# Optimization experiments

Hardware: AMD Instinct MI355X
Metric: run time of the kernel (lower is better)

Reference implementation:

```python
import jax, jax.numpy as jnp
import numpy as np

D_MODEL = 1024
D_OUT = 1024
N_EXPERTS = 8
TOP_K = 2


def setup_inputs() -> dict:
    key = jax.random.key(0)
    ks = jax.random.split(key, 5)
    b, t = 4, 4096
    inputs = jax.random.normal(ks[0], (b, t, D_MODEL), dtype=jnp.float32)
    # gate: Linear(input_dim, num_experts) -> weight (E, d), bias (E,)
    Wg = jax.random.normal(ks[1], (N_EXPERTS, D_MODEL), dtype=jnp.float32) / np.sqrt(D_MODEL)
    bg = jnp.zeros((N_EXPERTS,), dtype=jnp.float32)
    # experts: E x Linear(input_dim, output_dim) -> (E, d, f) and (E, f)
    We = jax.random.normal(ks[2], (N_EXPERTS, D_MODEL, D_OUT), dtype=jnp.float32) / np.sqrt(D_MODEL)
    be = jnp.zeros((N_EXPERTS, D_OUT), dtype=jnp.float32)
    return {"inputs": inputs, "Wg": Wg, "bg": bg, "We": We, "be": be}


def reference(inputs, Wg, bg, We, be):
    # gate logits: (b, t, E)
    gate_logits = jnp.einsum('btd,ed->bte', inputs, Wg) + bg
    # top-k per token (values descending, distinct indices) -> (b, t, k)
    topv, topi = jax.lax.top_k(gate_logits, TOP_K)
    gatew = jax.nn.sigmoid(topv).astype(inputs.dtype)            # (b, t, k)
    # scatter the k gate weights into a dense per-expert combine weight (b, t, E)
    onehot = jax.nn.one_hot(topi, N_EXPERTS, dtype=inputs.dtype)  # (b, t, k, E)
    combine = jnp.einsum('btk,btke->bte', gatew, onehot)          # (b, t, E)
    # per-expert linear outputs for all tokens: (b, t, E, f)
    expert_out = jnp.einsum('btd,edf->btef', inputs, We) + be
    # weighted combine over experts (unselected experts have weight 0)
    results = jnp.einsum('bte,btef->btf', combine, expert_out)
    return results
```

## Files before the change

kernel.cpp:

```cpp
#include <hip/hip_runtime.h>
#include <math.h>

#define DM 1024
#define DF 1024
#define NE 8
#define NBIN 16
#define MAXT 136
#define BM 128
#define BN 64
#define BKT 32
#define NT 32

typedef __bf16 bf16x8 __attribute__((ext_vector_type(8)));
typedef __bf16 bf16x4 __attribute__((ext_vector_type(4)));
typedef float floatx4 __attribute__((ext_vector_type(4)));

typedef const __attribute__((address_space(1))) unsigned int* gas_t;
typedef __attribute__((address_space(3))) unsigned int* las_t;

__device__ __forceinline__ void ld_lds16(const void* g, void* l) {
    __builtin_amdgcn_global_load_lds((gas_t)g, (las_t)l, 16, 0, 0);
}

#define WAITVM(N) asm volatile("s_waitcnt vmcnt(" #N ")" ::: "memory")
#define BARRIER() do { asm volatile("" ::: "memory"); \
                       __builtin_amdgcn_s_barrier(); \
                       asm volatile("" ::: "memory"); } while (0)


__global__ void convert_weT(const float* __restrict__ We, __bf16* __restrict__ WeT) {
    int n  = blockIdx.x * 256 + threadIdx.x;
    int kc = blockIdx.y * 8;
    int e  = blockIdx.z;
    const float* src = We + ((size_t)e << 20) + (size_t)kc * DF + n;
    bf16x8 v;
#pragma unroll
    for (int j = 0; j < 8; ++j) v[j] = (__bf16)src[(size_t)j * DF];
    *(bf16x8*)&WeT[((size_t)e << 20) + (size_t)n * DM + kc] = v;
}

__global__ void gate_kernel(const float4* __restrict__ X4, const float4* __restrict__ Wg4,
                            const float* __restrict__ bg, int* __restrict__ tok_e,
                            float* __restrict__ tok_w, __bf16* __restrict__ Xb, int T) {
    int wid  = threadIdx.x >> 6;
    int lane = threadIdx.x & 63;
    int t = blockIdx.x * 4 + wid;
    if (t >= T) return;
    float acc[NE] = {};
    float4 xs[4];
#pragma unroll
    for (int c = 0; c < 4; ++c) {
        float4 xv = X4[(size_t)t * 256 + c * 64 + lane];
        xs[c] = xv;
#pragma unroll
        for (int e = 0; e < NE; ++e) {
            float4 wv = Wg4[e * 256 + c * 64 + lane];
            acc[e] += xv.x * wv.x + xv.y * wv.y + xv.z * wv.z + xv.w * wv.w;
        }
    }
#pragma unroll
    for (int c = 0; c < 4; ++c) {
        bf16x4 v;
        v[0] = (__bf16)xs[c].x; v[1] = (__bf16)xs[c].y;
        v[2] = (__bf16)xs[c].z; v[3] = (__bf16)xs[c].w;
        *(bf16x4*)&Xb[(size_t)t * DM + c * 256 + lane * 4] = v;
    }
#pragma unroll
    for (int e = 0; e < NE; ++e) {
#pragma unroll
        for (int off = 32; off > 0; off >>= 1)
            acc[e] += __shfl_down(acc[e], off, 64);
    }
    if (lane == 0) {
        float l[NE];
#pragma unroll
        for (int e = 0; e < NE; ++e) l[e] = acc[e] + bg[e];
        int b0 = 0; float v0 = l[0];
        for (int e = 1; e < NE; ++e) if (l[e] > v0) { v0 = l[e]; b0 = e; }
        int b1 = -1; float v1 = -3.4e38f;
        for (int e = 0; e < NE; ++e) if (e != b0 && l[e] > v1) { v1 = l[e]; b1 = e; }
        tok_e[2 * t]     = b0;  tok_e[2 * t + 1] = b1;
        tok_w[2 * t]     = 1.f / (1.f + expf(-v0));
        tok_w[2 * t + 1] = 1.f / (1.f + expf(-v1));
    }
}

__global__ void hist_kernel(const int* __restrict__ tok_e, int* __restrict__ blk_cnt, int n) {
    int b = blockIdx.x, tid = threadIdx.x;
    int idx  = b * 256 + tid;
    int lane = tid & 63, w = tid >> 6;
    int bin = (idx < n) ? ((idx & 1) * NE + tok_e[idx]) : -1;
    __shared__ int wc[4][NBIN];
#pragma unroll
    for (int bx = 0; bx < NBIN; ++bx) {
        unsigned long long m = __ballot(bin == bx);
        if (lane == 0) wc[w][bx] = (int)__popcll(m);
    }
    __syncthreads();
    if (tid < NBIN) blk_cnt[b * NBIN + tid] = wc[0][tid] + wc[1][tid] + wc[2][tid] + wc[3][tid];
}

__global__ void scan_kernel(const int* __restrict__ blk_cnt, int* __restrict__ blk_base,
                            int4* __restrict__ wl, int* __restrict__ ntiles, int NB) {
    __shared__ int c[2048];
    __shared__ int tot[NBIN], base[NBIN];
    int tid = threadIdx.x;
    for (int i = tid; i < NB * NBIN; i += 256) c[i] = blk_cnt[i];
    __syncthreads();
    if (tid < NBIN) {
        int s = 0;
        for (int b = 0; b < NB; ++b) s += c[b * NBIN + tid];
        tot[tid] = s;
    }
    __syncthreads();
    if (tid == 0) {
        int s = 0;
        for (int b = 0; b < NBIN; ++b) { base[b] = s; s += tot[b]; }
    }
    __syncthreads();
    if (tid < NBIN) {
        int run = base[tid];
        for (int b = 0; b < NB; ++b) { int v = c[b * NBIN + tid]; c[b * NBIN + tid] = run; run += v; }
    }
    __syncthreads();
    for (int i = tid; i < NB * NBIN; i += 256) blk_base[i] = c[i];
    if (tid == 0) {
        for (int p = 0; p < 2; ++p) {
            int nt = 0;
            for (int e = 0; e < NE; ++e) {
                int bin = p * NE + e;
                int cnt = tot[bin], sg = base[bin];
                for (int r0 = 0; r0 < cnt; r0 += BM)
                    wl[p * MAXT + nt++] = make_int4(e, r0, sg, cnt);
            }
            ntiles[p] = nt;
        }
    }
}

__global__ void scatter_kernel(const int* __restrict__ tok_e, const float* __restrict__ tok_w,
                               const int* __restrict__ blk_base, int* __restrict__ gath_tok,
                               float* __restrict__ gath_w, int n) {
    int b = blockIdx.x, tid = threadIdx.x;
    int idx  = b * 256 + tid;
    int lane = tid & 63, w = tid >> 6;
    bool act = idx < n;
    int bin = act ? ((idx & 1) * NE + tok_e[idx]) : -1;
    __shared__ int wc[4][NBIN], wb[4][NBIN];
    int myrank = 0;
#pragma unroll
    for (int bx = 0; bx < NBIN; ++bx) {
        unsigned long long m = __ballot(bin == bx);
        if (lane == 0) wc[w][bx] = (int)__popcll(m);
        if (bin == bx) myrank = (int)__popcll(m & ((1ull << lane) - 1ull));
    }
    __syncthreads();
    if (tid < NBIN) {
        int run = blk_base[b * NBIN + tid];
#pragma unroll
        for (int wv = 0; wv < 4; ++wv) { wb[wv][tid] = run; run += wc[wv][tid]; }
    }
    __syncthreads();
    if (act) {
        int pos = wb[w][bin] + myrank;
        gath_tok[pos] = idx >> 1;
        gath_w[pos]   = tok_w[idx];
    }
}

template <bool ACC>
__global__ __launch_bounds__(256) void expert_gemm_mfma(
        const __bf16* __restrict__ Xb, const __bf16* __restrict__ WeT,
        const float* __restrict__ be, const int4* __restrict__ wl,
        const int* __restrict__ ntiles, const int* __restrict__ gtok,
        const float* __restrict__ gw, float* __restrict__ out) {
    int sw = (blockIdx.x & 7) * (2 * MAXT) + (blockIdx.x >> 3);
    int tix  = sw >> 4;
    int col0 = (sw & 15) * BN;
    if (tix >= ntiles[0]) return;
    int4 ent = wl[tix];
    int e = ent.x, row0 = ent.y, seg = ent.z, n_e = ent.w;

    __shared__ __align__(16) char smem[49152];
    __bf16* Asb = (__bf16*)smem;
    __bf16* Bsb = (__bf16*)(smem + 32768);
    float*  Cs  = (float*)smem;
    __shared__ int   s_tok[BM];
    __shared__ float s_w[BM];

    int tid = threadIdx.x;
    if (tid < BM) {
        int gr = row0 + tid;
        s_tok[tid] = (gr < n_e) ? gtok[seg + gr] : gtok[seg];
        s_w[tid]   = (gr < n_e) ? gw[seg + gr]   : 0.f;
    }
    __syncthreads();

    int lane = tid & 63, w = tid >> 6;
    int rsub = lane >> 2;
    int kc   = (lane & 3) ^ ((lane >> 3) & 3);

    const __bf16* aptr0 = Xb + (size_t)s_tok[w * 16 + rsub] * DM + kc * 8;
    const __bf16* aptr1 = Xb + (size_t)s_tok[(4 + w) * 16 + rsub] * DM + kc * 8;
    const __bf16* bptr  = WeT + ((size_t)e << 20)
                        + (size_t)(col0 + w * 16 + rsub) * DM + kc * 8;

    int wr  = (w >> 1) * 64;
    int wcc = (w & 1) * 32;
    int m16 = lane & 15, q4 = lane >> 4;
    int ccu = q4 ^ ((m16 >> 1) & 3);

    floatx4 acc[4][2] = {};

#define STAGE(B, KS) do { \
    ld_lds16(aptr0 + (KS) * BKT, Asb + (B) * 4096 + w * 512); \
    ld_lds16(aptr1 + (KS) * BKT, Asb + (B) * 4096 + (4 + w) * 512); \
    ld_lds16(bptr  + (KS) * BKT, Bsb + (B) * 2048 + w * 512); } while (0)

#define COMP(B) do { \
    bf16x8 af[4], bfr[2]; \
    _Pragma("unroll") \
    for (int i = 0; i < 4; ++i) \
        af[i] = *(const bf16x8*)&Asb[(B) * 4096 + (wr + i * 16 + m16) * 32 + ccu * 8]; \
    _Pragma("unroll") \
    for (int j = 0; j < 2; ++j) \
        bfr[j] = *(const bf16x8*)&Bsb[(B) * 2048 + (wcc + j * 16 + m16) * 32 + ccu * 8]; \
    _Pragma("unroll") \
    for (int i = 0; i < 4; ++i) \
        _Pragma("unroll") \
        for (int j = 0; j < 2; ++j) \
            acc[i][j] = __builtin_amdgcn_mfma_f32_16x16x32_bf16(af[i], bfr[j], acc[i][j], 0, 0, 0); \
    } while (0)

    STAGE(0, 0); STAGE(1, 1); STAGE(2, 2);
    WAITVM(6);
    BARRIER();

    for (int kk = 0; kk < NT - 4; kk += 4) {
        COMP(0); BARRIER(); STAGE(3, kk + 3); WAITVM(6); BARRIER();
        COMP(1); BARRIER(); STAGE(0, kk + 4); WAITVM(6); BARRIER();
        COMP(2); BARRIER(); STAGE(1, kk + 5); WAITVM(6); BARRIER();
        COMP(3); BARRIER(); STAGE(2, kk + 6); WAITVM(6); BARRIER();
    }
    COMP(0); BARRIER(); STAGE(3, NT - 1); WAITVM(6); BARRIER();
    COMP(1); BARRIER(); WAITVM(3); BARRIER();
    COMP(2); BARRIER(); WAITVM(0); BARRIER();
    COMP(3); BARRIER();

#undef STAGE
#undef COMP

#pragma unroll
    for (int j = 0; j < 2; ++j) {
#pragma unroll
        for (int i = 0; i < 4; ++i) {
#pragma unroll
            for (int rg = 0; rg < 4; ++rg) {
                int rl = wr + i * 16 + q4 * 4 + rg;
                int cl = wcc + j * 16 + m16;
                int cq = (cl >> 2) ^ (rl & 15);
                Cs[rl * 64 + cq * 4 + (cl & 3)] = acc[i][j][rg];
            }
        }
    }
    BARRIER();

#pragma unroll
    for (int rh = 0; rh < 2; ++rh) {
        int rr = w * 32 + rh * 16 + (lane >> 2);
        int gr2 = row0 + rr;
        if (gr2 < n_e) {
            int tok = s_tok[rr];
            float wgt = s_w[rr];
            float* orow = out + (size_t)tok * DF + col0;
            const float* brow = be + e * DF + col0;
#pragma unroll
            for (int kq = 0; kq < 4; ++kq) {
                int cq_log = kq * 4 + (lane & 3);
                int c4 = cq_log * 4;
                floatx4 v  = *(const floatx4*)&Cs[rr * 64 + ((cq_log ^ (rr & 15)) * 4)];
                floatx4 bv = *(const floatx4*)&brow[c4];
                floatx4 r;
#pragma unroll
                for (int z = 0; z < 4; ++z) r[z] = wgt * (v[z] + bv[z]);
                if (ACC) {
                    floatx4 o = *(const floatx4*)&orow[c4];
#pragma unroll
                    for (int z = 0; z < 4; ++z) r[z] += o[z];
                }
                *(floatx4*)&orow[c4] = r;
            }
        }
    }
}

extern "C" void kernel_launch(void* const* d_in, const int* in_sizes, int n_in,
                              void* d_out, int out_size, void* d_ws, size_t ws_size,
                              hipStream_t stream) {
    const float* x  = (const float*)d_in[0];
    const float* Wg = (const float*)d_in[1];
    const float* bg = (const float*)d_in[2];
    const float* We = (const float*)d_in[3];
    const float* be = (const float*)d_in[4];
    float* out = (float*)d_out;

    int T = in_sizes[0] / DM;
    int n_slots = 2 * T;
    int NB = (n_slots + 255) / 256;

    char* ws = (char*)d_ws;
    size_t xb_bytes  = (size_t)T * DM * 2;
    size_t weT_bytes = (size_t)NE * DM * DF * 2;
    __bf16* Xb  = (__bf16*)ws;
    __bf16* WeT = (__bf16*)(ws + xb_bytes);
    char* rt = ws + xb_bytes + weT_bytes;
    int*   ntiles    = (int*)(rt + 0);
    int4*  wl        = (int4*)(rt + 64);
    int*   blk_cnt   = (int*)(rt + 64 + 2 * MAXT * 16);
    int*   blk_base  = (int*)((char*)blk_cnt + (size_t)NB * NBIN * 4);
    int*   tok_e     = (int*)((char*)blk_base + (size_t)NB * NBIN * 4);
    float* tok_w     = (float*)((char*)tok_e + (size_t)n_slots * 4);
    int*   gath_tok  = (int*)((char*)tok_w + (size_t)n_slots * 4);
    float* gath_w    = (float*)((char*)gath_tok + (size_t)n_slots * 4);

    convert_weT<<<dim3(DF / 256, DM / 8, NE), 256, 0, stream>>>(We, WeT);
    gate_kernel<<<(T + 3) / 4, 256, 0, stream>>>((const float4*)x, (const float4*)Wg,
                                                 bg, tok_e, tok_w, Xb, T);
    hist_kernel<<<NB, 256, 0, stream>>>(tok_e, blk_cnt, n_slots);
    scan_kernel<<<1, 256, 0, stream>>>(blk_cnt, blk_base, wl, ntiles, NB);
    scatter_kernel<<<NB, 256, 0, stream>>>(tok_e, tok_w, blk_base, gath_tok, gath_w, n_slots);

    expert_gemm_mfma<false><<<MAXT * 16, 256, 0, stream>>>(Xb, WeT, be, wl, ntiles,
                                                           gath_tok, gath_w, out);
    expert_gemm_mfma<true><<<MAXT * 16, 256, 0, stream>>>(Xb, WeT, be, wl + MAXT, ntiles + 1,
                                                          gath_tok, gath_w, out);
}
```

Before: 310.9 us.

## Widen expert GEMM tile to 128x128 with triple-buffered LDS pipeline

Result: slower. 319.1 us (+2.6%).

```diff
diff --git a/kernel.cpp b/kernel.cpp
--- a/kernel.cpp
+++ b/kernel.cpp
@@ -7,7 +7,7 @@
 #define NBIN 16
 #define MAXT 136
 #define BM 128
-#define BN 64
+#define BN 128
 #define BKT 32
 #define NT 32
 
@@ -23,6 +23,7 @@
 }
 
 #define WAITVM(N) asm volatile("s_waitcnt vmcnt(" #N ")" ::: "memory")
+#define SCHEDB()  __builtin_amdgcn_sched_barrier(0)
 #define BARRIER() do { asm volatile("" ::: "memory"); \
                        __builtin_amdgcn_s_barrier(); \
                        asm volatile("" ::: "memory"); } while (0)
@@ -174,16 +175,16 @@
         const float* __restrict__ be, const int4* __restrict__ wl,
         const int* __restrict__ ntiles, const int* __restrict__ gtok,
         const float* __restrict__ gw, float* __restrict__ out) {
-    int sw = (blockIdx.x & 7) * (2 * MAXT) + (blockIdx.x >> 3);
-    int tix  = sw >> 4;
-    int col0 = (sw & 15) * BN;
+    int sw = (blockIdx.x & 7) * MAXT + (blockIdx.x >> 3);
+    int tix  = sw >> 3;
+    int col0 = (sw & 7) * BN;
     if (tix >= ntiles[0]) return;
     int4 ent = wl[tix];
     int e = ent.x, row0 = ent.y, seg = ent.z, n_e = ent.w;
 
     __shared__ __align__(16) char smem[49152];
     __bf16* Asb = (__bf16*)smem;
-    __bf16* Bsb = (__bf16*)(smem + 32768);
+    __bf16* Bsb = (__bf16*)(smem + 24576);
     float*  Cs  = (float*)smem;
     __shared__ int   s_tok[BM];
     __shared__ float s_w[BM];
@@ -202,95 +203,101 @@
 
     const __bf16* aptr0 = Xb + (size_t)s_tok[w * 16 + rsub] * DM + kc * 8;
     const __bf16* aptr1 = Xb + (size_t)s_tok[(4 + w) * 16 + rsub] * DM + kc * 8;
-    const __bf16* bptr  = WeT + ((size_t)e << 20)
+    const __bf16* bptr0 = WeT + ((size_t)e << 20)
                         + (size_t)(col0 + w * 16 + rsub) * DM + kc * 8;
+    const __bf16* bptr1 = WeT + ((size_t)e << 20)
+                        + (size_t)(col0 + 64 + w * 16 + rsub) * DM + kc * 8;
 
     int wr  = (w >> 1) * 64;
-    int wcc = (w & 1) * 32;
+    int wcc = (w & 1) * 64;
     int m16 = lane & 15, q4 = lane >> 4;
     int ccu = q4 ^ ((m16 >> 1) & 3);
 
-    floatx4 acc[4][2] = {};
+    floatx4 acc[4][4] = {};
 
 #define STAGE(B, KS) do { \
     ld_lds16(aptr0 + (KS) * BKT, Asb + (B) * 4096 + w * 512); \
     ld_lds16(aptr1 + (KS) * BKT, Asb + (B) * 4096 + (4 + w) * 512); \
-    ld_lds16(bptr  + (KS) * BKT, Bsb + (B) * 2048 + w * 512); } while (0)
+    ld_lds16(bptr0 + (KS) * BKT, Bsb + (B) * 4096 + w * 512); \
+    ld_lds16(bptr1 + (KS) * BKT, Bsb + (B) * 4096 + (4 + w) * 512); } while (0)
 
 #define COMP(B) do { \
-    bf16x8 af[4], bfr[2]; \
+    bf16x8 af[4], bfr[4]; \
     _Pragma("unroll") \
     for (int i = 0; i < 4; ++i) \
         af[i] = *(const bf16x8*)&Asb[(B) * 4096 + (wr + i * 16 + m16) * 32 + ccu * 8]; \
     _Pragma("unroll") \
-    for (int j = 0; j < 2; ++j) \
-        bfr[j] = *(const bf16x8*)&Bsb[(B) * 2048 + (wcc + j * 16 + m16) * 32 + ccu * 8]; \
+    for (int j = 0; j < 4; ++j) \
+        bfr[j] = *(const bf16x8*)&Bsb[(B) * 4096 + (wcc + j * 16 + m16) * 32 + ccu * 8]; \
     _Pragma("unroll") \
     for (int i = 0; i < 4; ++i) \
         _Pragma("unroll") \
-        for (int j = 0; j < 2; ++j) \
+        for (int j = 0; j < 4; ++j) \
             acc[i][j] = __builtin_amdgcn_mfma_f32_16x16x32_bf16(af[i], bfr[j], acc[i][j], 0, 0, 0); \
     } while (0)
 
-    STAGE(0, 0); STAGE(1, 1); STAGE(2, 2);
-    WAITVM(6);
+    STAGE(0, 0); STAGE(1, 1);
+    WAITVM(4); SCHEDB();
     BARRIER();
 
-    for (int kk = 0; kk < NT - 4; kk += 4) {
-        COMP(0); BARRIER(); STAGE(3, kk + 3); WAITVM(6); BARRIER();
-        COMP(1); BARRIER(); STAGE(0, kk + 4); WAITVM(6); BARRIER();
-        COMP(2); BARRIER(); STAGE(1, kk + 5); WAITVM(6); BARRIER();
-        COMP(3); BARRIER(); STAGE(2, kk + 6); WAITVM(6); BARRIER();
-    }
-    COMP(0); BARRIER(); STAGE(3, NT - 1); WAITVM(6); BARRIER();
-    COMP(1); BARRIER(); WAITVM(3); BARRIER();
-    COMP(2); BARRIER(); WAITVM(0); BARRIER();
-    COMP(3); BARRIER();
+    for (int kk = 0; kk < NT - 2; kk += 3) {
+        COMP(0); BARRIER(); STAGE(2, kk + 2); WAITVM(4); SCHEDB(); BARRIER();
+        COMP(1); BARRIER(); STAGE(0, kk + 3); WAITVM(4); SCHEDB(); BARRIER();
+        COMP(2); BARRIER(); STAGE(1, kk + 4); WAITVM(4); SCHEDB(); BARRIER();
+    }
+    COMP(0); WAITVM(0); SCHEDB(); BARRIER();
+    COMP(1);
+    BARRIER();
 
 #undef STAGE
 #undef COMP
 
 #pragma unroll
-    for (int j = 0; j < 2; ++j) {
-#pragma unroll
-        for (int i = 0; i < 4; ++i) {
-#pragma unroll
-            for (int rg = 0; rg < 4; ++rg) {
-                int rl = wr + i * 16 + q4 * 4 + rg;
-                int cl = wcc + j * 16 + m16;
-                int cq = (cl >> 2) ^ (rl & 15);
-                Cs[rl * 64 + cq * 4 + (cl & 3)] = acc[i][j][rg];
+    for (int r = 0; r < 2; ++r) {
+        if ((w & 1) == r) {
+#pragma unroll
+            for (int j = 0; j < 4; ++j) {
+#pragma unroll
+                for (int i = 0; i < 4; ++i) {
+#pragma unroll
+                    for (int rg = 0; rg < 4; ++rg) {
+                        int rl = wr + i * 16 + q4 * 4 + rg;
+                        int cl = j * 16 + m16;
+                        int cq = (cl >> 2) ^ (rl & 15);
+                        Cs[rl * 64 + cq * 4 + (cl & 3)] = acc[i][j][rg];
+                    }
+                }
             }
         }
-    }
-    BARRIER();
-
-#pragma unroll
-    for (int rh = 0; rh < 2; ++rh) {
-        int rr = w * 32 + rh * 16 + (lane >> 2);
-        int gr2 = row0 + rr;
-        if (gr2 < n_e) {
-            int tok = s_tok[rr];
-            float wgt = s_w[rr];
-            float* orow = out + (size_t)tok * DF + col0;
-            const float* brow = be + e * DF + col0;
-#pragma unroll
-            for (int kq = 0; kq < 4; ++kq) {
-                int cq_log = kq * 4 + (lane & 3);
-                int c4 = cq_log * 4;
-                floatx4 v  = *(const floatx4*)&Cs[rr * 64 + ((cq_log ^ (rr & 15)) * 4)];
-                floatx4 bv = *(const floatx4*)&brow[c4];
-                floatx4 r;
-#pragma unroll
-                for (int z = 0; z < 4; ++z) r[z] = wgt * (v[z] + bv[z]);
-                if (ACC) {
-                    floatx4 o = *(const floatx4*)&orow[c4];
-#pragma unroll
-                    for (int z = 0; z < 4; ++z) r[z] += o[z];
+        BARRIER();
+#pragma unroll
+        for (int rh = 0; rh < 2; ++rh) {
+            int rr = w * 32 + rh * 16 + (lane >> 2);
+            int gr2 = row0 + rr;
+            if (gr2 < n_e) {
+                int tok = s_tok[rr];
+                float wgt = s_w[rr];
+                float* orow = out + (size_t)tok * DF + col0 + r * 64;
+                const float* brow = be + e * DF + col0 + r * 64;
+#pragma unroll
+                for (int kq = 0; kq < 4; ++kq) {
+                    int cq_log = kq * 4 + (lane & 3);
+                    int c4 = cq_log * 4;
+                    floatx4 v  = *(const floatx4*)&Cs[rr * 64 + ((cq_log ^ (rr & 15)) * 4)];
+                    floatx4 bv = *(const floatx4*)&brow[c4];
+                    floatx4 rv;
+#pragma unroll
+                    for (int z = 0; z < 4; ++z) rv[z] = wgt * (v[z] + bv[z]);
+                    if (ACC) {
+                        floatx4 o = *(const floatx4*)&orow[c4];
+#pragma unroll
+                        for (int z = 0; z < 4; ++z) rv[z] += o[z];
+                    }
+                    *(floatx4*)&orow[c4] = rv;
                 }
-                *(floatx4*)&orow[c4] = r;
             }
         }
+        BARRIER();
     }
 }
 
@@ -330,8 +337,8 @@
     scan_kernel<<<1, 256, 0, stream>>>(blk_cnt, blk_base, wl, ntiles, NB);
     scatter_kernel<<<NB, 256, 0, stream>>>(tok_e, tok_w, blk_base, gath_tok, gath_w, n_slots);
 
-    expert_gemm_mfma<false><<<MAXT * 16, 256, 0, stream>>>(Xb, WeT, be, wl, ntiles,
-                                                           gath_tok, gath_w, out);
-    expert_gemm_mfma<true><<<MAXT * 16, 256, 0, stream>>>(Xb, WeT, be, wl + MAXT, ntiles + 1,
+    expert_gemm_mfma<false><<<MAXT * 8, 256, 0, stream>>>(Xb, WeT, be, wl, ntiles,
                                                           gath_tok, gath_w, out);
-}
+    expert_gemm_mfma<true><<<MAXT * 8, 256, 0, stream>>>(Xb, WeT, be, wl + MAXT, ntiles + 1,
+                                                         gath_tok, gath_w, out);
+}
```
